# Kernel optimization log

Measured on AMD Instinct MI355X. Metric: run time of the kernel, lower is better.

The kernel has to match this reference:

```python
import jax, jax.numpy as jnp
import numpy as np

B, C_IN, N_PTS = 16, 4, 4096
N_P, DIM = 32, 256
EPS = 1e-5


def conv1d(x, w, b):
    # 1x1 Conv1d: x (B,C,N), w (O,C), b (O)
    return jnp.einsum('bcn,oc->bon', x, w) + b[None, :, None]


def bn(x, g, be):
    # BatchNorm1d in training mode: batch statistics over (B, N)
    m = jnp.mean(x, axis=(0, 2), keepdims=True)
    v = jnp.var(x, axis=(0, 2), keepdims=True)
    return g[None, :, None] * (x - m) * jax.lax.rsqrt(v + EPS) + be[None, :, None]


def softpool(x, n_p=N_P):
    # x: (B, C, N). For each sorting channel c, take indices of its top n_p
    # points and gather ALL C feature channels at those points.
    _, idx = jax.lax.top_k(x, n_p)            # (B, C_sort, n_p) indices into N
    g = jax.vmap(lambda xb, ib: xb[:, ib])(x, idx)  # (B, C_feat, C_sort, n_p)
    return jnp.transpose(g, (0, 1, 3, 2))     # (B, C_feat, n_p, C_sort)


def _forward(x, w1, b1, g1, be1, w2, b2, g2, be2, w3, b3, g3, be3,
             w8, b8, w9, b9, w4, b4, g4, be4, w5, b5, g5, be5,
             w6, b6, g6, be6, w7, b7):
    h = jax.nn.relu(bn(conv1d(x, w1, b1), g1, be1))      # (B,64,N)
    pointfeat = h
    h = jax.nn.relu(bn(conv1d(h, w2, b2), g2, be2))      # (B,128,N)
    h = bn(conv1d(h, w3, b3), g3, be3)                   # (B,256,N)
    sp = softpool(h)                                     # (B,256,32,256)
    # conv8: Conv2d(256,256,(1,256)) -> (B,256,32)
    y = jnp.einsum('bchw,ocw->boh', sp, w8) + b8[None, :, None]
    # conv9: Conv2d(256,256,(32,1)) -> (B,256)
    y = jnp.einsum('bch,och->bo', y, w9) + b9[None, :]
    glob = jnp.broadcast_to(y[:, :, None], (x.shape[0], DIM, x.shape[2]))
    h = jnp.concatenate([glob, pointfeat], axis=1)       # (B,320,N)
    h = jax.nn.relu(bn(conv1d(h, w4, b4), g4, be4))      # (B,512,N)
    h = jax.nn.relu(bn(conv1d(h, w5, b5), g5, be5))      # (B,256,N)
    h = jax.nn.relu(bn(conv1d(h, w6, b6), g6, be6))      # (B,128,N)
    return jnp.tanh(conv1d(h, w7, b7))                   # (B,3,N)


def setup_inputs() -> dict:
    key = jax.random.key(0)
    ks = iter(jax.random.split(key, 64))
    def p(shape, scale=0.05):
        return (jax.random.normal(next(ks), shape, jnp.float32) * scale)
    inp = {}
    inp['x'] = jax.random.normal(next(ks), (B, C_IN, N_PTS), jnp.float32)
    for name, o, i in [('1', 64, 4), ('2', 128, 64), ('3', 256, 128),
                       ('4', 512, 320), ('5', 256, 512), ('6', 128, 256)]:
        inp['w' + name] = p((o, i))
        inp['b' + name] = p((o,))
        inp['g' + name] = jnp.ones((o,), jnp.float32)
        inp['be' + name] = jnp.zeros((o,), jnp.float32)
    inp['w7'] = p((3, 128)); inp['b7'] = p((3,))
    inp['w8'] = p((DIM, DIM, DIM)); inp['b8'] = p((DIM,))
    inp['w9'] = p((DIM, DIM, N_P)); inp['b9'] = p((DIM,))
    return inp


def reference(x, w1, b1, g1, be1, w2, b2, g2, be2, w3, b3, g3, be3,
              w4, b4, g4, be4, w5, b5, g5, be5, w6, b6, g6, be6,
              w7, b7, w8, b8, w9, b9):
    return _forward(x, w1, b1, g1, be1, w2, b2, g2, be2, w3, b3, g3, be3,
                    w8, b8, w9, b9, w4, b4, g4, be4, w5, b5, g5, be5,
                    w6, b6, g6, be6, w7, b7)
```

## Files before the change

kernel.cpp:

```cpp
#include <hip/hip_runtime.h>
#include <cstdint>
#include <cstddef>

#define NPTS 4096
#define BATCH 16

typedef unsigned int uint32;
typedef unsigned short u16;

typedef __attribute__((ext_vector_type(8))) short short8;
typedef __attribute__((ext_vector_type(16))) float float16;

__device__ __forceinline__ u16 f2bf(float f) {
  uint32 u = __float_as_uint(f);
  u = (u + 0x7fffu + ((u >> 16) & 1u)) >> 16;
  return (u16)u;
}
__device__ __forceinline__ float bf2f(u16 h) {
  return __uint_as_float(((uint32)h) << 16);
}

__global__ __launch_bounds__(256) void conv_gemm(
    const float* __restrict__ act, const float* __restrict__ wt,
    const float* __restrict__ rowbias, const float* __restrict__ obias,
    const float* __restrict__ inScale, const float* __restrict__ inShift,
    float* __restrict__ out, float* __restrict__ partials, int C, int O)
{
  __shared__ float As[16][68];
  __shared__ float Ws[16][68];
  __shared__ float redS[64][17];
  __shared__ float redQ[64][17];
  const int b  = blockIdx.z;
  const int o0 = blockIdx.y * 64;
  const int n0 = blockIdx.x * 64;
  const int t  = threadIdx.x;
  const int tx = t & 15, ty = t >> 4;
  float acc[4][4] = {};
  const float* actb = act + ((size_t)b * C) * NPTS;

  for (int k0 = 0; k0 < C; k0 += 16) {
    const int r  = ty;
    const int cs = tx * 4;
    const int k  = k0 + r;
    float4 av = make_float4(0.f, 0.f, 0.f, 0.f);
    if (k < C) {
      av = *(const float4*)(actb + (size_t)k * NPTS + n0 + cs);
      if (inScale) {
        const float scv = inScale[k], shv = inShift[k];
        av.x = fmaxf(fmaf(av.x, scv, shv), 0.f);
        av.y = fmaxf(fmaf(av.y, scv, shv), 0.f);
        av.z = fmaxf(fmaf(av.z, scv, shv), 0.f);
        av.w = fmaxf(fmaf(av.w, scv, shv), 0.f);
      }
    }
    *(float4*)&As[r][cs] = av;

    float4 wv = make_float4(0.f, 0.f, 0.f, 0.f);
    if (k < C) {
      const float* wp = wt + (size_t)k * O;
      const int o = o0 + cs;
      if (o + 3 < O) {
        wv = *(const float4*)&wp[o];
      } else {
        float tmp[4] = {0.f, 0.f, 0.f, 0.f};
        for (int j = 0; j < 4; ++j) if (o + j < O) tmp[j] = wp[o + j];
        wv = make_float4(tmp[0], tmp[1], tmp[2], tmp[3]);
      }
    }
    *(float4*)&Ws[r][cs] = wv;
    __syncthreads();

    const int kmax = (C - k0 < 16) ? (C - k0) : 16;
    for (int kk = 0; kk < kmax; ++kk) {
      float4 a = *(float4*)&As[kk][tx * 4];
      float4 w = *(float4*)&Ws[kk][ty * 4];
      acc[0][0] += w.x * a.x; acc[0][1] += w.x * a.y; acc[0][2] += w.x * a.z; acc[0][3] += w.x * a.w;
      acc[1][0] += w.y * a.x; acc[1][1] += w.y * a.y; acc[1][2] += w.y * a.z; acc[1][3] += w.y * a.w;
      acc[2][0] += w.z * a.x; acc[2][1] += w.z * a.y; acc[2][2] += w.z * a.z; acc[2][3] += w.z * a.w;
      acc[3][0] += w.w * a.x; acc[3][1] += w.w * a.y; acc[3][2] += w.w * a.z; acc[3][3] += w.w * a.w;
    }
    __syncthreads();
  }

  float s[4], q[4];
  for (int i = 0; i < 4; ++i) {
    const int o = o0 + ty * 4 + i;
    s[i] = 0.f; q[i] = 0.f;
    if (o >= O) continue;
    float base = 0.f;
    if (rowbias) base  = rowbias[(size_t)b * O + o];
    if (obias)   base += obias[o];
    float4 v = make_float4(acc[i][0] + base, acc[i][1] + base, acc[i][2] + base, acc[i][3] + base);
    *(float4*)&out[((size_t)b * O + o) * NPTS + n0 + tx * 4] = v;
    s[i] = v.x + v.y + v.z + v.w;
    q[i] = v.x * v.x + v.y * v.y + v.z * v.z + v.w * v.w;
  }

  if (partials) {
    for (int i = 0; i < 4; ++i) { redS[ty * 4 + i][tx] = s[i]; redQ[ty * 4 + i][tx] = q[i]; }
    __syncthreads();
    if (t < 64) {
      float a = 0.f;
      for (int j = 0; j < 16; ++j) a += redS[t][j];
      partials[((size_t)b * O + o0 + t) * 64 + blockIdx.x] = a;
    } else if (t < 128) {
      float a = 0.f;
      for (int j = 0; j < 16; ++j) a += redQ[t - 64][j];
      partials[(size_t)BATCH * O * 64 + ((size_t)b * O + o0 + t - 64) * 64 + blockIdx.x] = a;
    }
  }
}


__global__ __launch_bounds__(256) void conv1_f64(const float* __restrict__ x,
                                                 const float* __restrict__ w1,
                                                 float* __restrict__ h1f,
                                                 double* __restrict__ psd) {
  const int c = blockIdx.x, b = blockIdx.y;
  const double wa = (double)w1[c * 4 + 0], wb = (double)w1[c * 4 + 1];
  const double wc = (double)w1[c * 4 + 2], wd = (double)w1[c * 4 + 3];
  const float* xb = x + (size_t)b * 4 * NPTS;
  float* dst = h1f + ((size_t)b * 64 + c) * NPTS;
  double s = 0.0, q = 0.0;
  for (int n = threadIdx.x; n < NPTS; n += 256) {
    double v = wa * (double)xb[n] + wb * (double)xb[NPTS + n]
             + wc * (double)xb[2 * NPTS + n] + wd * (double)xb[3 * NPTS + n];
    dst[n] = (float)v;
    s += v; q += v * v;
  }
  __shared__ double ls[4], lq[4];
  for (int off = 32; off; off >>= 1) { s += __shfl_down(s, off, 64); q += __shfl_down(q, off, 64); }
  const int wid = threadIdx.x >> 6;
  if ((threadIdx.x & 63) == 0) { ls[wid] = s; lq[wid] = q; }
  __syncthreads();
  if (threadIdx.x == 0) {
    s = ls[0] + ls[1] + ls[2] + ls[3];
    q = lq[0] + lq[1] + lq[2] + lq[3];
    psd[(size_t)c * 16 + b] = s;
    psd[(size_t)64 * 16 + (size_t)c * 16 + b] = q;
  }
}

__global__ __launch_bounds__(256) void bn_finalize_f64(const double* __restrict__ psd,
                                                       const float* __restrict__ g,
                                                       const float* __restrict__ be,
                                                       double* __restrict__ scd, double* __restrict__ shd,
                                                       float* __restrict__ scf, float* __restrict__ shf,
                                                       int NT) {
  const int c = blockIdx.x;
  const int t = threadIdx.x;
  const double* p2 = psd + (size_t)gridDim.x * NT;
  const int k = (NT + 255) / 256;
  double s = 0.0, q = 0.0;
  for (int i = t * k; i < (t + 1) * k && i < NT; ++i) {
    s += psd[(size_t)c * NT + i];
    q += p2[(size_t)c * NT + i];
  }
  __shared__ double ss[256], qq[256];
  ss[t] = s; qq[t] = q;
  __syncthreads();
  if (t == 0) {
    double S = 0.0, Q = 0.0;
    for (int i = 0; i < 256; ++i) { S += ss[i]; Q += qq[i]; }
    const double m   = S * (1.0 / 65536.0);
    const double var = Q * (1.0 / 65536.0) - m * m;
    const double sc  = (double)g[c] / sqrt(var + 1e-5);
    const double sh  = (double)be[c] - m * sc;
    if (scd) { scd[c] = sc; shd[c] = sh; }
    scf[c] = (float)sc;
    shf[c] = (float)sh;
  }
}

__global__ __launch_bounds__(256) void pack_wtf64(const float* __restrict__ src,
                                                  double* __restrict__ dst,
                                                  int O, int C) {
  int i = blockIdx.x * 256 + threadIdx.x;
  if (i >= O * C) return;
  int c = i / O, o = i - c * O;
  dst[(size_t)c * O + o] = (double)src[(size_t)o * C + c];
}

__global__ __launch_bounds__(256) void conv2_f64v(
    const float* __restrict__ x, const float* __restrict__ w1,
    const double* __restrict__ w2t,
    const double* __restrict__ scd1, const double* __restrict__ shd1,
    double* __restrict__ h2d, double* __restrict__ psd)
{
  __shared__ double Bs[64][65];
  __shared__ double Ws[16][132];
  const int nb = blockIdx.x, b = blockIdx.y;
  const int n0 = nb * 64;
  const int t = threadIdx.x;
  const float* xb = x + (size_t)b * 4 * NPTS + n0;
  for (int i = t; i < 64 * 64; i += 256) {
    const int c1 = i >> 6, n = i & 63;
    double v = (double)w1[c1 * 4 + 0] * (double)xb[n]
             + (double)w1[c1 * 4 + 1] * (double)xb[NPTS + n]
             + (double)w1[c1 * 4 + 2] * (double)xb[2 * NPTS + n]
             + (double)w1[c1 * 4 + 3] * (double)xb[3 * NPTS + n];
    v = v * scd1[c1] + shd1[c1];
    Bs[c1][n] = v > 0.0 ? v : 0.0;
  }
  const int tx = t & 15, ty = t >> 4;
  double acc[8][4] = {};
  for (int ch = 0; ch < 4; ++ch) {
    __syncthreads();
    {
      const int r = t >> 4, oo = (t & 15) * 8;
      const double* srcw = w2t + (size_t)(ch * 16 + r) * 128 + oo;
#pragma unroll
      for (int j = 0; j < 8; ++j) Ws[r][oo + j] = srcw[j];
    }
    __syncthreads();
#pragma unroll
    for (int kk = 0; kk < 16; ++kk) {
      double a[8], bv[4];
#pragma unroll
      for (int j = 0; j < 8; ++j) a[j] = Ws[kk][ty * 8 + j];
#pragma unroll
      for (int j = 0; j < 4; ++j) bv[j] = Bs[ch * 16 + kk][tx * 4 + j];
#pragma unroll
      for (int i = 0; i < 8; ++i)
#pragma unroll
        for (int j = 0; j < 4; ++j) acc[i][j] = fma(a[i], bv[j], acc[i][j]);
    }
  }
  const size_t hb = (size_t)b * 128 * NPTS;
#pragma unroll
  for (int i = 0; i < 8; ++i) {
    const int o = ty * 8 + i;
    double s = 0.0, q = 0.0;
#pragma unroll
    for (int j = 0; j < 4; ++j) {
      const double v = acc[i][j];
      h2d[hb + (size_t)o * NPTS + n0 + tx * 4 + j] = v;
      s += v; q += v * v;
    }
#pragma unroll
    for (int m = 1; m < 16; m <<= 1) { s += __shfl_xor(s, m, 64); q += __shfl_xor(q, m, 64); }
    if (tx == 0) {
      psd[(size_t)o * 1024 + b * 64 + nb] = s;
      psd[(size_t)128 * 1024 + (size_t)o * 1024 + b * 64 + nb] = q;
    }
  }
}

__global__ __launch_bounds__(256) void conv3_f64v(
    const double* __restrict__ h2d, const double* __restrict__ w3t,
    const double* __restrict__ scd2, const double* __restrict__ shd2,
    double* __restrict__ h3d, double* __restrict__ psd)
{
  __shared__ double Bs[16][132];
  __shared__ double Ws[16][68];
  const int nb = blockIdx.x, og = blockIdx.y, b = blockIdx.z;
  const int n0 = nb * 128, o0 = og * 64;
  const int t = threadIdx.x;
  const int tx = t & 31, ty = t >> 5;
  const double* h2b = h2d + (size_t)b * 128 * NPTS;
  double acc[8][4] = {};
  for (int ch = 0; ch < 8; ++ch) {
    __syncthreads();
    {
      const int r = t >> 4, nn = (t & 15) * 8;
      const int c2 = ch * 16 + r;
      const double sc = scd2[c2], sh = shd2[c2];
      const double* srcr = h2b + (size_t)c2 * NPTS + n0 + nn;
#pragma unroll
      for (int j = 0; j < 8; ++j) {
        double v = srcr[j] * sc + sh;
        Bs[r][nn + j] = v > 0.0 ? v : 0.0;
      }
    }
    {
      const int r = t >> 4, oo = (t & 15) * 4;
      const double* srcw = w3t + (size_t)(ch * 16 + r) * 256 + o0 + oo;
#pragma unroll
      for (int j = 0; j < 4; ++j) Ws[r][oo + j] = srcw[j];
    }
    __syncthreads();
#pragma unroll
    for (int kk = 0; kk < 16; ++kk) {
      double a[8], bv[4];
#pragma unroll
      for (int j = 0; j < 8; ++j) a[j] = Ws[kk][ty * 8 + j];
#pragma unroll
      for (int j = 0; j < 4; ++j) bv[j] = Bs[kk][tx * 4 + j];
#pragma unroll
      for (int i = 0; i < 8; ++i)
#pragma unroll
        for (int j = 0; j < 4; ++j) acc[i][j] = fma(a[i], bv[j], acc[i][j]);
    }
  }
#pragma unroll
  for (int i = 0; i < 8; ++i) {
    const int o = o0 + ty * 8 + i;
    double s = 0.0, q = 0.0;
#pragma unroll
    for (int j = 0; j < 4; ++j) {
      const double v = acc[i][j];
      h3d[((size_t)b * 256 + o) * NPTS + n0 + tx * 4 + j] = v;
      s += v; q += v * v;
    }
#pragma unroll
    for (int m = 1; m < 32; m <<= 1) { s += __shfl_xor(s, m, 64); q += __shfl_xor(q, m, 64); }
    if (tx == 0) {
      psd[(size_t)o * 512 + b * 32 + nb] = s;
      psd[(size_t)256 * 512 + (size_t)o * 512 + b * 32 + nb] = q;
    }
  }
}

__global__ __launch_bounds__(256) void pack_wmfma(const float* __restrict__ src,
                                                  u16* __restrict__ ph, u16* __restrict__ pl,
                                                  int O, int Ctot, int cOff, int Csub) {
  int i = blockIdx.x * 256 + threadIdx.x;
  if (i >= O * Csub) return;
  const int KS = Csub >> 4;
  int j    = i & 7;
  int lj   = (i >> 3) & 63;
  int mtks = i >> 9;
  int ks   = mtks % KS;
  int mt   = mtks / KS;
  int o = mt * 32 + (lj & 31);
  int c = ks * 16 + (lj >> 5) * 8 + j;
  float v = src[(size_t)o * Ctot + cOff + c];
  u16 h = f2bf(v);
  ph[i] = h;
  pl[i] = f2bf(v - bf2f(h));
}

__global__ __launch_bounds__(256) void conv_mfma(
    const float* __restrict__ act, const u16* __restrict__ wh, const u16* __restrict__ wl,
    const float* __restrict__ rowbias,
    const float* __restrict__ inScale, const float* __restrict__ inShift,
    float* __restrict__ out, float* __restrict__ ps, int C, int O)
{
  __shared__ u16 Bh[2][4096];
  __shared__ u16 Bl[2][4096];
  const int b  = blockIdx.z;
  const int o0 = blockIdx.y * 128;
  const int n0 = blockIdx.x * 128;
  const int t  = threadIdx.x;
  const int l  = t & 63, wva = t >> 6;
  const int mt = blockIdx.y * 4 + wva;
  const int KS = C >> 4;
  const int NCH = C >> 5;
  const float* actb = act + ((size_t)b * C) * NPTS;

  float16 acc[4];
#pragma unroll
  for (int ns = 0; ns < 4; ++ns)
#pragma unroll
    for (int r = 0; r < 16; ++r) acc[ns][r] = 0.f;

  const int cq = t >> 5;
  const int nq = t & 31;
  const int nn = n0 + nq * 4;
  const int ksl = cq >> 2, oct = (cq >> 1) & 1, j0 = (cq & 1) * 4;

  float va[4][4];
  float4 scv = make_float4(1.f,1.f,1.f,1.f), shv = make_float4(0.f,0.f,0.f,0.f);

  auto loadChunk = [&](int ch) {
    const int cb = ch * 32 + cq * 4;
#pragma unroll
    for (int i2 = 0; i2 < 4; ++i2) {
      float4 v4 = *(const float4*)(actb + (size_t)(cb + i2) * NPTS + nn);
      va[i2][0] = v4.x; va[i2][1] = v4.y; va[i2][2] = v4.z; va[i2][3] = v4.w;
    }
    if (inScale) {
      scv = *(const float4*)&inScale[cb];
      shv = *(const float4*)&inShift[cb];
    }
  };
  auto applyBN = [&]() {
    if (!inScale) return;
#pragma unroll
    for (int d = 0; d < 4; ++d) {
      va[0][d] = fmaxf(fmaf(va[0][d], scv.x, shv.x), 0.f);
      va[1][d] = fmaxf(fmaf(va[1][d], scv.y, shv.y), 0.f);
      va[2][d] = fmaxf(fmaf(va[2][d], scv.z, shv.z), 0.f);
      va[3][d] = fmaxf(fmaf(va[3][d], scv.w, shv.w), 0.f);
    }
  };
  auto convWrite = [&](int buf) {
#pragma unroll
    for (int d = 0; d < 4; ++d) {
      const int nrel = nq * 4 + d;
      const int ns = nrel >> 5, li = nrel & 31;
      u16 h0 = f2bf(va[0][d]), h1 = f2bf(va[1][d]), h2 = f2bf(va[2][d]), h3 = f2bf(va[3][d]);
      u16 q0 = f2bf(va[0][d] - bf2f(h0));
      u16 q1 = f2bf(va[1][d] - bf2f(h1));
      u16 q2 = f2bf(va[2][d] - bf2f(h2));
      u16 q3 = f2bf(va[3][d] - bf2f(h3));
      const int idx = ((ksl * 4 + ns) * 64 + oct * 32 + li) * 8 + j0;
      *(ushort4*)&Bh[buf][idx] = make_ushort4(h0, h1, h2, h3);
      *(ushort4*)&Bl[buf][idx] = make_ushort4(q0, q1, q2, q3);
    }
  };

  loadChunk(0);
  applyBN();
  convWrite(0);
  __syncthreads();

  for (int ch = 0; ch < NCH; ++ch) {
    const size_t abase = (((size_t)mt * KS + ch * 2) * 64 + (size_t)l) * 8;
    short8 AH0 = *(const short8*)(wh + abase);
    short8 AH1 = *(const short8*)(wh + abase + 512);
    short8 AL0 = *(const short8*)(wl + abase);
    short8 AL1 = *(const short8*)(wl + abase + 512);
    const bool more = (ch + 1 < NCH);
    if (more) loadChunk(ch + 1);

    const u16* bh = Bh[ch & 1];
    const u16* bl = Bl[ch & 1];
#pragma unroll
    for (int ns = 0; ns < 4; ++ns) {
      short8 BH0 = *(const short8*)&bh[((0 * 4 + ns) * 64 + l) * 8];
      short8 BL0 = *(const short8*)&bl[((0 * 4 + ns) * 64 + l) * 8];
      acc[ns] = __builtin_amdgcn_mfma_f32_32x32x16_bf16(AL0, BH0, acc[ns], 0, 0, 0);
      acc[ns] = __builtin_amdgcn_mfma_f32_32x32x16_bf16(AH0, BL0, acc[ns], 0, 0, 0);
      acc[ns] = __builtin_amdgcn_mfma_f32_32x32x16_bf16(AH0, BH0, acc[ns], 0, 0, 0);
      short8 BH1 = *(const short8*)&bh[((4 + ns) * 64 + l) * 8];
      short8 BL1 = *(const short8*)&bl[((4 + ns) * 64 + l) * 8];
      acc[ns] = __builtin_amdgcn_mfma_f32_32x32x16_bf16(AL1, BH1, acc[ns], 0, 0, 0);
      acc[ns] = __builtin_amdgcn_mfma_f32_32x32x16_bf16(AH1, BL1, acc[ns], 0, 0, 0);
      acc[ns] = __builtin_amdgcn_mfma_f32_32x32x16_bf16(AH1, BH1, acc[ns], 0, 0, 0);
    }
    if (more) { applyBN(); convWrite((ch + 1) & 1); }
    __syncthreads();
  }

  const int col = l & 31, half = l >> 5;
  float sv[16], sq[16];
#pragma unroll
  for (int r = 0; r < 16; ++r) {
    const int o = o0 + wva * 32 + (r & 3) + 8 * (r >> 2) + 4 * half;
    const float base = rowbias ? rowbias[(size_t)b * O + o] : 0.f;
    float s = 0.f, q = 0.f;
#pragma unroll
    for (int ns = 0; ns < 4; ++ns) {
      float val = acc[ns][r] + base;
      out[((size_t)b * O + o) * NPTS + n0 + ns * 32 + col] = val;
      s += val; q += val * val;
    }
    sv[r] = s; sq[r] = q;
  }
  if (ps) {
#pragma unroll
    for (int r = 0; r < 16; ++r) {
#pragma unroll
      for (int m = 1; m < 32; m <<= 1) {
        sv[r] += __shfl_xor(sv[r], m, 64);
        sq[r] += __shfl_xor(sq[r], m, 64);
      }
    }
    if (col == 0) {
#pragma unroll
      for (int r = 0; r < 16; ++r) {
        const int o = o0 + wva * 32 + (r & 3) + 8 * (r >> 2) + 4 * half;
        ps[((size_t)b * O + o) * 32 + blockIdx.x] = sv[r];
        ps[(size_t)BATCH * O * 32 + ((size_t)b * O + o) * 32 + blockIdx.x] = sq[r];
      }
    }
  }
}

__global__ __launch_bounds__(256) void bn_finalize(const float* __restrict__ ps,
                                                   const float* __restrict__ g, const float* __restrict__ be,
                                                   float* __restrict__ scale, float* __restrict__ shift,
                                                   int O, int NT) {
  const int c = blockIdx.x;
  const int total = BATCH * NT;
  const float* p2 = ps + (size_t)BATCH * O * NT;
  const int t = threadIdx.x;
  float s = 0.f, q = 0.f;
  for (int e = t; e < total; e += 256) {
    const int b = e / NT, nt = e - b * NT;
    const size_t a = ((size_t)b * O + c) * NT + nt;
    s += ps[a];
    q += p2[a];
  }
#pragma unroll
  for (int m = 32; m; m >>= 1) {
    s += __shfl_down(s, m, 64);
    q += __shfl_down(q, m, 64);
  }
  __shared__ float lsS[4], lsQ[4];
  const int wid = t >> 6;
  if ((t & 63) == 0) { lsS[wid] = s; lsQ[wid] = q; }
  __syncthreads();
  if (t == 0) {
    s = lsS[0] + lsS[1] + lsS[2] + lsS[3];
    q = lsQ[0] + lsQ[1] + lsQ[2] + lsQ[3];
    const float inv = 1.f / 65536.f;
    float m   = s * inv;
    float var = q * inv - m * m;
    float sc  = g[c] * rsqrtf(var + 1e-5f);
    scale[c] = sc;
    shift[c] = be[c] - m * sc;
  }
}

__global__ __launch_bounds__(256) void topk_kernel(const double* __restrict__ h3,
                                                   int* __restrict__ idxp) {
  __shared__ double wvv[4];
  __shared__ int    wvi[4];
  __shared__ int    bcI;
  const int c = blockIdx.x, b = blockIdx.y;
  const double* src = h3 + ((size_t)b * 256 + c) * NPTS;
  const int t = threadIdx.x;
  double v[16];
  double bv = -1e308; int bi = NPTS;
#pragma unroll
  for (int s = 0; s < 16; ++s) {
    v[s] = src[t + 256 * s];
    if (v[s] > bv) { bv = v[s]; bi = t + 256 * s; }
  }
  int* dst = idxp + ((size_t)b * 256 + c) * 32;
  for (int r = 0; r < 32; ++r) {
    double rv = bv; int ri = bi;
#pragma unroll
    for (int off = 32; off; off >>= 1) {
      double ov = __shfl_down(rv, off, 64);
      int    oi = __shfl_down(ri, off, 64);
      if (ov > rv || (ov == rv && oi < ri)) { rv = ov; ri = oi; }
    }
    if ((t & 63) == 0) { wvv[t >> 6] = rv; wvi[t >> 6] = ri; }
    __syncthreads();
    if (t == 0) {
      for (int k = 1; k < 4; ++k)
        if (wvv[k] > rv || (wvv[k] == rv && wvi[k] < ri)) { rv = wvv[k]; ri = wvi[k]; }
      dst[r] = ri;
      bcI = ri;
    }
    __syncthreads();
    const int wi_ = bcI;
    if ((wi_ & 255) == t) {
      const int slot = wi_ >> 8;
#pragma unroll
      for (int s = 0; s < 16; ++s) if (s == slot) v[s] = -1e308;
      bv = -1e308; bi = NPTS;
#pragma unroll
      for (int s = 0; s < 16; ++s) if (v[s] > bv) { bv = v[s]; bi = t + 256 * s; }
    }
  }
}

__global__ __launch_bounds__(256) void transpose_h3(const double* __restrict__ h3,
                                                    float* __restrict__ h3T,
                                                    const float* __restrict__ sc,
                                                    const float* __restrict__ sh) {
  __shared__ double tile[32][33];
  const int b = blockIdx.z;
  const int n0 = blockIdx.x * 32, c0 = blockIdx.y * 32;
  const int tx = threadIdx.x & 31, ty = threadIdx.x >> 5;
  const double* src = h3 + (size_t)b * 256 * NPTS;
  for (int j = 0; j < 4; ++j)
    tile[ty + j * 8][tx] = src[(size_t)(c0 + ty + j * 8) * NPTS + n0 + tx];
  __syncthreads();
  float* dst = h3T + (size_t)b * NPTS * 256;
  const float scv = sc[c0 + tx], shv = sh[c0 + tx];
  for (int j = 0; j < 4; ++j)
    dst[(size_t)(n0 + ty + j * 8) * 256 + c0 + tx] = fmaf((float)tile[tx][ty + j * 8], scv, shv);
}

__global__ __launch_bounds__(256) void transpack_w8(const float* __restrict__ w8,
                                                    u16* __restrict__ w8h, u16* __restrict__ w8l) {
  __shared__ float tile[64][65];
  const int m0 = blockIdx.x * 64, w0 = blockIdx.y * 64;
  const int tx = threadIdx.x & 63, ty = threadIdx.x >> 6;
#pragma unroll
  for (int j = 0; j < 16; ++j)
    tile[ty + j * 4][tx] = w8[(size_t)(m0 + ty + j * 4) * 256 + w0 + tx];
  __syncthreads();
  const int m = m0 + tx;
  const int o = m >> 8, c = m & 255;
  const int mt = (o >> 5) & 7;
  const int lane = (o & 31) + ((c >> 3) & 1) * 32;
  const int ks = (c >> 4) & 15;
  const int jj = c & 7;
#pragma unroll
  for (int j = 0; j < 16; ++j) {
    const int w = w0 + ty + j * 4;
    float v = tile[tx][ty + j * 4];
    size_t f = ((((size_t)w * 8 + mt) * 16 + ks) * 64 + lane) * 8 + jj;
    u16 h = f2bf(v);
    w8h[f] = h;
    w8l[f] = f2bf(v - bf2f(h));
  }
}

#define Y8N (BATCH * 256 * 32)
__global__ __launch_bounds__(256, 1) void conv8_mfma(
    const float* __restrict__ h3T, const u16* __restrict__ w8h,
    const u16* __restrict__ w8l, const int* __restrict__ idxp,
    float* __restrict__ y8p)
{
  __shared__ u16 G[2][8192];
  const int wg = blockIdx.x;
  const int oq = blockIdx.y;
  const int bg = blockIdx.z;
  const int t  = threadIdx.x;
  const int l  = t & 63, wv = t >> 6;
  const int mt = oq * 4 + wv;

  float16 accH[4], accL[4];
  for (int i = 0; i < 4; ++i)
    for (int r = 0; r < 16; ++r) { accH[i][r] = 0.f; accL[i][r] = 0.f; }

  short8 ah[16], al[16];
  const int hrow  = t >> 3;
  const int cbase = (t & 7) * 32;
  float4 g4[8];

  auto issueG = [&](int step) {
    int wi = step >> 2, bi = step & 3;
    int w = wg * 8 + wi;
    int b = bg * 4 + bi;
    int n = idxp[((size_t)b * 256 + w) * 32 + hrow];
    const float* src = h3T + ((size_t)b * NPTS + n) * 256 + cbase;
#pragma unroll
    for (int j = 0; j < 8; ++j) g4[j] = *(const float4*)&src[j * 4];
  };
  auto writeG = [&](int buf) {
#pragma unroll
    for (int a = 0; a < 4; ++a) {
      int c8 = (cbase >> 3) + a;
      int ks = c8 >> 1;
      int lp = hrow + (c8 & 1) * 32;
      float4 v0 = g4[a * 2], v1 = g4[a * 2 + 1];
      uint32 u0 = (uint32)f2bf(v0.x) | ((uint32)f2bf(v0.y) << 16);
      uint32 u1 = (uint32)f2bf(v0.z) | ((uint32)f2bf(v0.w) << 16);
      uint32 u2 = (uint32)f2bf(v1.x) | ((uint32)f2bf(v1.y) << 16);
      uint32 u3 = (uint32)f2bf(v1.z) | ((uint32)f2bf(v1.w) << 16);
      *(uint4*)&G[buf][((size_t)ks * 64 + lp) * 8] = make_uint4(u0, u1, u2, u3);
    }
  };

  issueG(0); writeG(0);
  __syncthreads();

  for (int wi = 0; wi < 8; ++wi) {
    const int w = wg * 8 + wi;
    {
      const size_t base = (((size_t)w * 8 + mt) * 16) * 512 + (size_t)l * 8;
#pragma unroll
      for (int ks = 0; ks < 16; ++ks) {
        ah[ks] = *(const short8*)(w8h + base + ks * 512);
        al[ks] = *(const short8*)(w8l + base + ks * 512);
      }
    }
#pragma unroll
    for (int bi = 0; bi < 4; ++bi) {
      const int step = wi * 4 + bi;
      const int cur = bi & 1;
      if (step < 31) issueG(step + 1);
      const u16* Gc = G[cur];
#pragma unroll
      for (int ks = 0; ks < 16; ++ks) {
        short8 bf = *(const short8*)&Gc[((size_t)ks * 64 + l) * 8];
        accH[bi] = __builtin_amdgcn_mfma_f32_32x32x16_bf16(ah[ks], bf, accH[bi], 0, 0, 0);
        accL[bi] = __builtin_amdgcn_mfma_f32_32x32x16_bf16(al[ks], bf, accL[bi], 0, 0, 0);
      }
      if (step < 31) writeG(1 - cur);
      __syncthreads();
    }
  }

  const int h = l & 31;
  const int rbase = oq * 128 + wv * 32 + 4 * (l >> 5);
#pragma unroll
  for (int bi = 0; bi < 4; ++bi) {
    int b = bg * 4 + bi;
    float* dst = y8p + ((size_t)(wg * BATCH + b) * 256) * 32;
#pragma unroll
    for (int r = 0; r < 16; ++r) {
      int o = rbase + (r & 3) + 8 * (r >> 2);
      dst[(size_t)o * 32 + h] = accH[bi][r] + accL[bi][r];
    }
  }
}

__global__ __launch_bounds__(256) void y8_reduce(const float* __restrict__ y8p,
                                                 const float* __restrict__ b8,
                                                 float* __restrict__ y8) {
  int i = blockIdx.x * 256 + threadIdx.x;
  float s = b8[(i >> 5) & 255];
#pragma unroll
  for (int p = 0; p < 32; ++p) s += y8p[(size_t)p * Y8N + i];
  y8[i] = s;
}

__global__ __launch_bounds__(256) void conv9_kernel(const float* __restrict__ y8,
                                                    const float* __restrict__ w9,
                                                    const float* __restrict__ b9,
                                                    float* __restrict__ y9) {
  const int o = blockIdx.x, b = blockIdx.y;
  const float* yb = y8 + (size_t)b * 8192;
  const float* wo = w9 + (size_t)o * 8192;
  float s = 0.f;
  for (int i = threadIdx.x * 4; i < 8192; i += 1024) {
    float4 v = *(const float4*)&yb[i];
    float4 u = *(const float4*)&wo[i];
    s += v.x * u.x + v.y * u.y + v.z * u.z + v.w * u.w;
  }
  for (int off = 32; off; off >>= 1) s += __shfl_down(s, off, 64);
  __shared__ float ls[4];
  const int wid = threadIdx.x >> 6;
  if ((threadIdx.x & 63) == 0) ls[wid] = s;
  __syncthreads();
  if (threadIdx.x == 0) y9[(size_t)b * 256 + o] = ls[0] + ls[1] + ls[2] + ls[3] + b9[o];
}

__global__ __launch_bounds__(256) void cvec_kernel(const float* __restrict__ y9,
                                                   const float* __restrict__ w4,
                                                   float* __restrict__ cvec) {
  int tid = blockIdx.x * 256 + threadIdx.x;
  if (tid >= BATCH * 512) return;
  const int b = tid >> 9, o = tid & 511;
  const float* row = w4 + (size_t)o * 320;
  const float* yb  = y9 + (size_t)b * 256;
  float s = 0.f;
  for (int c = 0; c < 256; c += 4) {
    float4 u = *(const float4*)&row[c];
    s += u.x * yb[c] + u.y * yb[c + 1] + u.z * yb[c + 2] + u.w * yb[c + 3];
  }
  cvec[(size_t)b * 512 + o] = s;
}

__global__ __launch_bounds__(256) void transpose_w(const float* __restrict__ src,
                                                   float* __restrict__ dst,
                                                   int O, int Ctot, int cOff, int Csub) {
  int i = blockIdx.x * 256 + threadIdx.x;
  if (i >= O * Csub) return;
  int c = i / O, o = i - c * O;
  dst[(size_t)c * O + o] = src[(size_t)o * Ctot + cOff + c];
}

__global__ __launch_bounds__(256) void tanh_out(const float* __restrict__ raw,
                                                float* __restrict__ out) {
  int i = blockIdx.x * 256 + threadIdx.x;
  if (i < BATCH * 3 * NPTS) out[i] = tanhf(raw[i]);
}

extern "C" void kernel_launch(void* const* d_in, const int* in_sizes, int n_in,
                              void* d_out, int out_size, void* d_ws, size_t ws_size,
                              hipStream_t stream) {
  (void)in_sizes; (void)n_in; (void)ws_size; (void)out_size;
  const float* x   = (const float*)d_in[0];
  const float* w1  = (const float*)d_in[1];
  const float* g1  = (const float*)d_in[3];
  const float* be1 = (const float*)d_in[4];
  const float* w2  = (const float*)d_in[5];
  const float* g2  = (const float*)d_in[7];
  const float* be2 = (const float*)d_in[8];
  const float* w3  = (const float*)d_in[9];
  const float* g3  = (const float*)d_in[11];
  const float* be3 = (const float*)d_in[12];
  const float* w4  = (const float*)d_in[13];
  const float* g4  = (const float*)d_in[15];
  const float* be4 = (const float*)d_in[16];
  const float* w5  = (const float*)d_in[17];
  const float* g5  = (const float*)d_in[19];
  const float* be5 = (const float*)d_in[20];
  const float* w6  = (const float*)d_in[21];
  const float* g6  = (const float*)d_in[23];
  const float* be6 = (const float*)d_in[24];
  const float* w7  = (const float*)d_in[25];
  const float* b7  = (const float*)d_in[26];
  const float* w8  = (const float*)d_in[27];
  const float* b8  = (const float*)d_in[28];
  const float* w9  = (const float*)d_in[29];
  const float* b9  = (const float*)d_in[30];

  char* ws = (char*)d_ws;
  size_t off = 0;
  auto alloc = [&](size_t bytes) -> void* {
    void* p = ws + off;
    off += (bytes + 255) & ~(size_t)255;
    return p;
  };
  float* Q1  = (float*)alloc((size_t)BATCH * 64  * NPTS * 4);
  float* Q2  = (float*)alloc((size_t)BATCH * 128 * NPTS * 4);
  float* Q3  = (float*)alloc((size_t)BATCH * 256 * NPTS * 4);
  float* Q4  = (float*)alloc((size_t)BATCH * 256 * NPTS * 4);
  float* Q5  = (float*)alloc((size_t)BATCH * 256 * NPTS * 4);
  int*   idx  = (int*)alloc((size_t)BATCH * 256 * 32 * 4);
  float* y8   = (float*)alloc((size_t)Y8N * 4);
  float* y9   = (float*)alloc((size_t)BATCH * 256 * 4);
  float* cvec = (float*)alloc((size_t)BATCH * 512 * 4);
  float* ps   = (float*)alloc((size_t)2 * BATCH * 512 * 32 * 4);
  double* psd = (double*)alloc((size_t)2 * 256 * 1024 * 8);
  float* scb  = (float*)alloc((size_t)6 * 1024 * 4);
  double* scdb = (double*)alloc((size_t)1024 * 8);
  float* w7t  = (float*)alloc(128 * 3 * 4);
  u16* ph4 = (u16*)alloc(512 * 64  * 2);  u16* pl4 = (u16*)alloc(512 * 64  * 2);
  u16* ph5 = (u16*)alloc(256 * 512 * 2);  u16* pl5 = (u16*)alloc(256 * 512 * 2);
  u16* ph6 = (u16*)alloc(128 * 256 * 2);  u16* pl6 = (u16*)alloc(128 * 256 * 2);
  double* w2t = (double*)alloc((size_t)64 * 128 * 8);
  double* w3t = (double*)alloc((size_t)128 * 256 * 8);

  double* h2d = (double*)Q3;
  double* h3d = (double*)Q4;
  u16*   w8h = (u16*)Q4;
  u16*   w8l = (u16*)Q4 + (size_t)16777216;
  float* y8p = Q2;
  float* h4  = Q2;
  float* h5  = Q5;
  float* h6  = Q2;

  float* sc[6]; float* sh[6];
  for (int i = 0; i < 6; ++i) { sc[i] = scb + i * 1024; sh[i] = scb + i * 1024 + 512; }
  double* scd1 = scdb;        double* shd1 = scdb + 64;
  double* scd2 = scdb + 128;  double* shd2 = scdb + 256;

  transpose_w<<<(128 * 3 + 255) / 256, 256, 0, stream>>>(w7, w7t, 3, 128, 0, 128);
  pack_wmfma<<<(512 * 64  + 255) / 256, 256, 0, stream>>>(w4, ph4, pl4, 512, 320, 256, 64);
  pack_wmfma<<<(256 * 512 + 255) / 256, 256, 0, stream>>>(w5, ph5, pl5, 256, 512, 0,   512);
  pack_wmfma<<<(128 * 256 + 255) / 256, 256, 0, stream>>>(w6, ph6, pl6, 128, 256, 0,   256);
  pack_wtf64<<<(128 * 64 + 255) / 256,  256, 0, stream>>>(w2, w2t, 128, 64);
  pack_wtf64<<<(256 * 128 + 255) / 256, 256, 0, stream>>>(w3, w3t, 256, 128);

  conv1_f64<<<dim3(64, BATCH), 256, 0, stream>>>(x, w1, Q1, psd);
  bn_finalize_f64<<<64, 256, 0, stream>>>(psd, g1, be1, scd1, shd1, sc[0], sh[0], 16);
  conv2_f64v<<<dim3(64, BATCH), 256, 0, stream>>>(x, w1, w2t, scd1, shd1, h2d, psd);
  bn_finalize_f64<<<128, 256, 0, stream>>>(psd, g2, be2, scd2, shd2, sc[1], sh[1], 1024);
  conv3_f64v<<<dim3(32, 4, BATCH), 256, 0, stream>>>(h2d, w3t, scd2, shd2, h3d, psd);
  bn_finalize_f64<<<256, 256, 0, stream>>>(psd, g3, be3, nullptr, nullptr, sc[2], sh[2], 512);

  topk_kernel<<<dim3(256, BATCH), 256, 0, stream>>>(h3d, idx);
  transpose_h3<<<dim3(NPTS / 32, 8, BATCH), 256, 0, stream>>>(h3d, Q3, sc[2], sh[2]);

  transpack_w8<<<dim3(1024, 4), 256, 0, stream>>>(w8, w8h, w8l);

  conv8_mfma<<<dim3(32, 2, 4), 256, 0, stream>>>(Q3, w8h, w8l, idx, y8p);
  y8_reduce<<<Y8N / 256, 256, 0, stream>>>(y8p, b8, y8);
  conv9_kernel<<<dim3(256, BATCH), 256, 0, stream>>>(y8, w9, b9, y9);
  cvec_kernel<<<(BATCH * 512 + 255) / 256, 256, 0, stream>>>(y9, w4, cvec);

  conv_mfma<<<dim3(32, 4, BATCH), 256, 0, stream>>>(Q1, ph4, pl4, cvec, sc[0], sh[0], h4, ps, 64, 512);
  bn_finalize<<<512, 256, 0, stream>>>(ps, g4, be4, sc[3], sh[3], 512, 32);
  conv_mfma<<<dim3(32, 2, BATCH), 256, 0, stream>>>(h4, ph5, pl5, nullptr, sc[3], sh[3], h5, ps, 512, 256);
  bn_finalize<<<256, 256, 0, stream>>>(ps, g5, be5, sc[4], sh[4], 256, 32);
  conv_mfma<<<dim3(32, 1, BATCH), 256, 0, stream>>>(h5, ph6, pl6, nullptr, sc[4], sh[4], h6, ps, 256, 128);
  bn_finalize<<<128, 256, 0, stream>>>(ps, g6, be6, sc[5], sh[5], 128, 32);
  conv_gemm<<<dim3(64, 1, BATCH), 256, 0, stream>>>(h6, w7t, nullptr, b7, sc[5], sh[5], Q1, nullptr, 128, 3);
  tanh_out<<<(BATCH * 3 * NPTS) / 256, 256, 0, stream>>>(Q1, (float*)d_out);
}
```

Before: 897.3 us.

## Make top-k per-wave independent then merge four sorted lists

```diff
diff --git a/kernel.cpp b/kernel.cpp
--- a/kernel.cpp
+++ b/kernel.cpp
@@ -506,45 +506,65 @@
 
 __global__ __launch_bounds__(256) void topk_kernel(const double* __restrict__ h3,
                                                    int* __restrict__ idxp) {
-  __shared__ double wvv[4];
-  __shared__ int    wvi[4];
-  __shared__ int    bcI;
+  __shared__ double wlV[4][32];
+  __shared__ int    wlI[4][32];
   const int c = blockIdx.x, b = blockIdx.y;
   const double* src = h3 + ((size_t)b * 256 + c) * NPTS;
   const int t = threadIdx.x;
+  const int l = t & 63, w = t >> 6;
+  const int base = w * 1024;
+
   double v[16];
-  double bv = -1e308; int bi = NPTS;
-#pragma unroll
-  for (int s = 0; s < 16; ++s) {
-    v[s] = src[t + 256 * s];
-    if (v[s] > bv) { bv = v[s]; bi = t + 256 * s; }
-  }
-  int* dst = idxp + ((size_t)b * 256 + c) * 32;
+  double bv; int bs;
+  {
+    v[0] = src[base + l];
+    bv = v[0]; bs = 0;
+#pragma unroll
+    for (int s = 1; s < 16; ++s) {
+      v[s] = src[base + s * 64 + l];
+      if (v[s] > bv) { bv = v[s]; bs = s; }
+    }
+  }
+
   for (int r = 0; r < 32; ++r) {
-    double rv = bv; int ri = bi;
+    double rv = bv; int ri = base + bs * 64 + l;
 #pragma unroll
     for (int off = 32; off; off >>= 1) {
       double ov = __shfl_down(rv, off, 64);
       int    oi = __shfl_down(ri, off, 64);
       if (ov > rv || (ov == rv && oi < ri)) { rv = ov; ri = oi; }
     }
-    if ((t & 63) == 0) { wvv[t >> 6] = rv; wvi[t >> 6] = ri; }
-    __syncthreads();
-    if (t == 0) {
-      for (int k = 1; k < 4; ++k)
-        if (wvv[k] > rv || (wvv[k] == rv && wvi[k] < ri)) { rv = wvv[k]; ri = wvi[k]; }
-      dst[r] = ri;
-      bcI = ri;
-    }
-    __syncthreads();
-    const int wi_ = bcI;
-    if ((wi_ & 255) == t) {
-      const int slot = wi_ >> 8;
+    const double wv_ = __shfl(rv, 0, 64);
+    const int    wi_ = __shfl(ri, 0, 64);
+    if (l == 0) { wlV[w][r] = wv_; wlI[w][r] = wi_; }
+    if ((wi_ & 63) == l) {
+      const int slot = (wi_ >> 6) & 15;
 #pragma unroll
       for (int s = 0; s < 16; ++s) if (s == slot) v[s] = -1e308;
-      bv = -1e308; bi = NPTS;
-#pragma unroll
-      for (int s = 0; s < 16; ++s) if (v[s] > bv) { bv = v[s]; bi = t + 256 * s; }
+      bv = v[0]; bs = 0;
+#pragma unroll
+      for (int s = 1; s < 16; ++s) if (v[s] > bv) { bv = v[s]; bs = s; }
+    }
+  }
+  __syncthreads();
+
+  if (t < 4) {
+    int* dst = idxp + ((size_t)b * 256 + c) * 32;
+    int cp = 0;
+    double cv = wlV[t][0]; int ci = wlI[t][0];
+    for (int r = 0; r < 32; ++r) {
+      double mv = cv; int mi = ci;
+      double ov; int oi;
+      ov = __shfl_xor(mv, 1, 64); oi = __shfl_xor(mi, 1, 64);
+      if (ov > mv || (ov == mv && oi < mi)) { mv = ov; mi = oi; }
+      ov = __shfl_xor(mv, 2, 64); oi = __shfl_xor(mi, 2, 64);
+      if (ov > mv || (ov == mv && oi < mi)) { mv = ov; mi = oi; }
+      if (t == 0) dst[r] = mi;
+      if (mi == ci) {
+        ++cp;
+        if (cp < 32) { cv = wlV[t][cp]; ci = wlI[t][cp]; }
+        else         { cv = -1e308;    ci = NPTS + t; }
+      }
     }
   }
 }
```

After: 908.9 us. Within noise of the previous version (+1.3%).

## Rewrite top-k as per-wave selection on packed keys with a final merge

Applied to the files above, without the earlier changes.

```diff
diff --git a/kernel.cpp b/kernel.cpp
--- a/kernel.cpp
+++ b/kernel.cpp
@@ -6,6 +6,7 @@
 #define BATCH 16
 
 typedef unsigned int uint32;
+typedef unsigned long long u64;
 typedef unsigned short u16;
 
 typedef __attribute__((ext_vector_type(8))) short short8;
@@ -506,45 +507,68 @@
 
 __global__ __launch_bounds__(256) void topk_kernel(const double* __restrict__ h3,
                                                    int* __restrict__ idxp) {
-  __shared__ double wvv[4];
-  __shared__ int    wvi[4];
-  __shared__ int    bcI;
+  __shared__ u64 wl[4][32];
   const int c = blockIdx.x, b = blockIdx.y;
   const double* src = h3 + ((size_t)b * 256 + c) * NPTS;
   const int t = threadIdx.x;
-  double v[16];
-  double bv = -1e308; int bi = NPTS;
+  const int l = t & 63, w = t >> 6;
+  const int base = w * 1024;
+
+  u64 k[16];
+  u64 bk = 0;
 #pragma unroll
   for (int s = 0; s < 16; ++s) {
-    v[s] = src[t + 256 * s];
-    if (v[s] > bv) { bv = v[s]; bi = t + 256 * s; }
-  }
-  int* dst = idxp + ((size_t)b * 256 + c) * 32;
+    const int ri = base + s * 64 + l;
+    u64 u = (u64)__double_as_longlong(src[ri]);
+    u64 m = ((long long)u < 0) ? ~u : (u | 0x8000000000000000ULL);
+    m = (m & ~0xFFFULL) | (u64)(4095 - ri);
+    k[s] = m;
+    if (m > bk) bk = m;
+  }
+
   for (int r = 0; r < 32; ++r) {
-    double rv = bv; int ri = bi;
-#pragma unroll
-    for (int off = 32; off; off >>= 1) {
-      double ov = __shfl_down(rv, off, 64);
-      int    oi = __shfl_down(ri, off, 64);
-      if (ov > rv || (ov == rv && oi < ri)) { rv = ov; ri = oi; }
-    }
-    if ((t & 63) == 0) { wvv[t >> 6] = rv; wvi[t >> 6] = ri; }
-    __syncthreads();
-    if (t == 0) {
-      for (int k = 1; k < 4; ++k)
-        if (wvv[k] > rv || (wvv[k] == rv && wvi[k] < ri)) { rv = wvv[k]; ri = wvi[k]; }
-      dst[r] = ri;
-      bcI = ri;
-    }
-    __syncthreads();
-    const int wi_ = bcI;
-    if ((wi_ & 255) == t) {
-      const int slot = wi_ >> 8;
-#pragma unroll
-      for (int s = 0; s < 16; ++s) if (s == slot) v[s] = -1e308;
-      bv = -1e308; bi = NPTS;
-#pragma unroll
-      for (int s = 0; s < 16; ++s) if (v[s] > bv) { bv = v[s]; bi = t + 256 * s; }
+    u64 m = bk;
+#pragma unroll
+    for (int off = 1; off < 64; off <<= 1) {
+      u64 o = __shfl_xor((unsigned long long)m, off, 64);
+      if (o > m) m = o;
+    }
+    if (l == 0) wl[w][r] = m;
+    const int ri = 4095 - (int)(m & 0xFFF);
+    if ((ri & 63) == l) {
+      const int slot = (ri >> 6) & 15;
+#pragma unroll
+      for (int s = 0; s < 16; ++s) if (s == slot) k[s] = 0;
+      u64 m0 = k[0] > k[1] ? k[0] : k[1];
+      u64 m1 = k[2] > k[3] ? k[2] : k[3];
+      u64 m2 = k[4] > k[5] ? k[4] : k[5];
+      u64 m3 = k[6] > k[7] ? k[6] : k[7];
+      u64 m4 = k[8] > k[9] ? k[8] : k[9];
+      u64 m5 = k[10] > k[11] ? k[10] : k[11];
+      u64 m6 = k[12] > k[13] ? k[12] : k[13];
+      u64 m7 = k[14] > k[15] ? k[14] : k[15];
+      m0 = m0 > m1 ? m0 : m1;  m2 = m2 > m3 ? m2 : m3;
+      m4 = m4 > m5 ? m4 : m5;  m6 = m6 > m7 ? m6 : m7;
+      m0 = m0 > m2 ? m0 : m2;  m4 = m4 > m6 ? m4 : m6;
+      bk = m0 > m4 ? m0 : m4;
+    }
+  }
+  __syncthreads();
+
+  if (t < 4) {
+    int* dst = idxp + ((size_t)b * 256 + c) * 32;
+    int cp = 0;
+    u64 cv = wl[t][0];
+    for (int r = 0; r < 32; ++r) {
+      u64 mv = cv;
+      u64 ov;
+      ov = __shfl_xor((unsigned long long)mv, 1, 64); if (ov > mv) mv = ov;
+      ov = __shfl_xor((unsigned long long)mv, 2, 64); if (ov > mv) mv = ov;
+      if (t == 0) dst[r] = 4095 - (int)(mv & 0xFFF);
+      if (mv == cv) {
+        ++cp;
+        cv = (cp < 32) ? wl[t][cp] : 0;
+      }
     }
   }
 }
```

After: 863.0 us. 1.04x faster.
